# Performance work log

Measured on AMD Instinct MI355X. Metric: run time of the kernel, lower is better.

Reference implementation:

```python
import jax, jax.numpy as jnp
import numpy as np

N_NODES = 50000
N_EDGES = 600000
IN_C = 128
HID = 128
OUT_C = 32
N_GRAPHS = 64


def setup_inputs() -> dict:
    key = jax.random.key(0)
    ks = jax.random.split(key, 12)
    x = jax.random.normal(ks[0], (N_NODES, IN_C), dtype=jnp.float32)
    edge_index = jax.random.randint(ks[1], (2, N_EDGES), 0, N_NODES, dtype=jnp.int64)
    batch = jnp.sort(jax.random.randint(ks[2], (N_NODES,), 0, N_GRAPHS, dtype=jnp.int64))
    s1 = 1.0 / np.sqrt(IN_C)
    s2 = 1.0 / np.sqrt(HID)
    # SAGEConv: out = lin_l(mean_neighbors) + lin_r(x); lin_l has bias, lin_r has none
    W1l = jax.random.uniform(ks[3], (HID, IN_C), minval=-s1, maxval=s1, dtype=jnp.float32)
    b1 = jax.random.uniform(ks[4], (HID,), minval=-s1, maxval=s1, dtype=jnp.float32)
    W1r = jax.random.uniform(ks[5], (HID, IN_C), minval=-s1, maxval=s1, dtype=jnp.float32)
    W2l = jax.random.uniform(ks[6], (HID, HID), minval=-s2, maxval=s2, dtype=jnp.float32)
    b2 = jax.random.uniform(ks[7], (HID,), minval=-s2, maxval=s2, dtype=jnp.float32)
    W2r = jax.random.uniform(ks[8], (HID, HID), minval=-s2, maxval=s2, dtype=jnp.float32)
    Wlin = jax.random.uniform(ks[9], (OUT_C, HID), minval=-s2, maxval=s2, dtype=jnp.float32)
    blin = jax.random.uniform(ks[10], (OUT_C,), minval=-s2, maxval=s2, dtype=jnp.float32)
    return {"x": x, "edge_index": edge_index, "batch": batch,
            "W1l": W1l, "b1": b1, "W1r": W1r,
            "W2l": W2l, "b2": b2, "W2r": W2r,
            "Wlin": Wlin, "blin": blin}


def _sage_conv(x, src, dst, Wl, bl, Wr):
    # mean aggregation of source-node features onto destination nodes
    msg_sum = jax.ops.segment_sum(x[src], dst, num_segments=N_NODES)  # [N, d]
    deg = jax.ops.segment_sum(jnp.ones((src.shape[0],), x.dtype), dst, num_segments=N_NODES)
    mean = msg_sum / jnp.maximum(deg, 1.0)[:, None]
    return mean @ Wl.T + bl + x @ Wr.T


def reference(x, edge_index, batch, W1l, b1, W1r, W2l, b2, W2r, Wlin, blin):
    src, dst = edge_index[0], edge_index[1]
    h = jax.nn.relu(_sage_conv(x, src, dst, W1l, b1, W1r))
    h = jax.nn.relu(_sage_conv(h, src, dst, W2l, b2, W2r))
    # global mean pool over graph ids
    gsum = jax.ops.segment_sum(h, batch, num_segments=N_GRAPHS)        # [G, HID]
    cnt = jax.ops.segment_sum(jnp.ones((h.shape[0],), h.dtype), batch, num_segments=N_GRAPHS)
    pooled = gsum / jnp.maximum(cnt, 1.0)[:, None]
    return pooled @ Wlin.T + blin
```

## Files before the change

### kernel.cpp

```cpp
#include <hip/hip_runtime.h>
#include <hip/hip_fp16.h>

#define N_NODES 50000
#define N_EDGES 600000
#define N_GRAPHS 64
#define HID 128
#define OUT_C 32

#define N_SCAN_BLOCKS ((N_NODES + 255) / 256)
#define SCAN_FLAG 0x40000000

typedef __attribute__((ext_vector_type(8))) _Float16 half8;
typedef __attribute__((ext_vector_type(4))) float f32x4;

#define ZERO_INTS (2 * N_NODES + N_SCAN_BLOCKS)

__global__ __launch_bounds__(256) void prep_kernel(
    const float* __restrict__ x, const int* __restrict__ batch,
    const float* __restrict__ W1l, const float* __restrict__ W1r,
    const float* __restrict__ W2l, const float* __restrict__ W2r,
    __half* __restrict__ xh, __half* __restrict__ Wt1, __half* __restrict__ Wt2,
    int* __restrict__ zero_base, int* __restrict__ gstart) {
    const int b = blockIdx.x;
    const int t = threadIdx.x;
    const int gtid = b * 256 + t;
    const int gsz = gridDim.x * 256;
    for (int i = gtid; i < ZERO_INTS; i += gsz) zero_base[i] = 0;

    for (int i = gtid; i <= N_NODES; i += gsz) {
        if (i == 0) {
            int b1 = batch[0];
            for (int g = 0; g <= b1; ++g) gstart[g] = 0;
        } else if (i == N_NODES) {
            int b0 = batch[N_NODES - 1];
            for (int g = b0 + 1; g <= N_GRAPHS; ++g) gstart[g] = N_NODES;
        } else {
            int b0 = batch[i - 1], b1 = batch[i];
            for (int g = b0 + 1; g <= b1; ++g) gstart[g] = i;
        }
    }

    if (b < 16) {
        for (int i = gtid; i < 65536; i += 4096) {
            int which = i >> 15;
            int j = i & 32767;
            int n = j >> 8, k = j & 255;
            const float* Wl = which ? W2l : W1l;
            const float* Wr = which ? W2r : W1r;
            float a = (k < 128) ? Wl[n * 128 + k] : Wr[n * 128 + (k - 128)];
            (which ? Wt2 : Wt1)[j] = __float2half(a);
        }
    } else {
        int i = ((b - 16) * 256 + t) * 4;
        if (i < N_NODES * 128) {
            float4 v = *(const float4*)(x + i);
            __half2 a = __floats2half2_rn(v.x, v.y);
            __half2 c = __floats2half2_rn(v.z, v.w);
            uint2 st;
            st.x = *(const unsigned int*)&a;
            st.y = *(const unsigned int*)&c;
            *(uint2*)(xh + i) = st;
        }
    }
}

__global__ void deg_kernel(const int* __restrict__ dst, int* __restrict__ deg, int E) {
    int e = blockIdx.x * 256 + threadIdx.x;
    if (e < E) atomicAdd(&deg[dst[e]], 1);
}

__global__ __launch_bounds__(256) void scan_fused(
    const int* __restrict__ deg, int* __restrict__ bsum,
    int* __restrict__ rowptr, float* __restrict__ invdeg) {
    __shared__ int s[256];
    const int b = blockIdx.x;
    const int t = threadIdx.x;
    const int idx = b * 256 + t;
    const int v = (idx < N_NODES) ? deg[idx] : 0;
    s[t] = v;
    __syncthreads();
    for (int off = 1; off < 256; off <<= 1) {
        int u = (t >= off) ? s[t - off] : 0;
        __syncthreads();
        s[t] += u;
        __syncthreads();
    }
    const int incl = s[t];
    if (t == 255) atomicExch(&bsum[b], incl | SCAN_FLAG);

    int pv = 0;
    if (t < b) {
        int w;
        do { w = atomicAdd(&bsum[t], 0); } while (!(w & SCAN_FLAG));
        pv = w & ~SCAN_FLAG;
    }
    __syncthreads();
    s[t] = pv;
    __syncthreads();
    for (int off = 128; off > 0; off >>= 1) {
        if (t < off) s[t] += s[t + off];
        __syncthreads();
    }
    const int boffs = s[0];

    if (idx < N_NODES) {
        rowptr[idx] = boffs + incl - v;
        invdeg[idx] = 1.0f / fmaxf((float)v, 1.0f);
    }
    if (b == N_SCAN_BLOCKS - 1 && t == 255) rowptr[N_NODES] = boffs + incl;
}

__global__ void fill_kernel(const int* __restrict__ src, const int* __restrict__ dst,
                            const int* __restrict__ rowptr, int* __restrict__ cursor,
                            int* __restrict__ eidx, int E) {
    int e = blockIdx.x * 256 + threadIdx.x;
    if (e < E) {
        int d = dst[e];
        int pos = atomicAdd(&cursor[d], 1);
        eidx[rowptr[d] + pos] = src[e];
    }
}

#define AGG8(vv, aa, ab) { aa.x += (float)vv[0]; aa.y += (float)vv[1]; \
                           aa.z += (float)vv[2]; aa.w += (float)vv[3]; \
                           ab.x += (float)vv[4]; ab.y += (float)vv[5]; \
                           ab.z += (float)vv[6]; ab.w += (float)vv[7]; }

__global__ __launch_bounds__(256) void aggregate_f16(
    const __half* __restrict__ feat16, const int* __restrict__ rowptr,
    const int* __restrict__ eidx, const float* __restrict__ invdeg,
    __half* __restrict__ mean16) {
    const int wave = threadIdx.x >> 6;
    const int lane = threadIdx.x & 63;
    const int nh   = lane >> 4;
    const int sub  = lane & 15;
    const int node = blockIdx.x * 16 + wave * 4 + nh;
    const bool act = (node < N_NODES);
    int beg = 0, end = 0;
    if (act) { beg = rowptr[node]; end = rowptr[node + 1]; }
    const size_t coff = (size_t)sub * 8;

    float4 a0 = {0.f,0.f,0.f,0.f}, b0 = {0.f,0.f,0.f,0.f};
    float4 a1 = {0.f,0.f,0.f,0.f}, b1 = {0.f,0.f,0.f,0.f};
    float4 a2 = {0.f,0.f,0.f,0.f}, b2 = {0.f,0.f,0.f,0.f};
    float4 a3 = {0.f,0.f,0.f,0.f}, b3 = {0.f,0.f,0.f,0.f};
    int i = beg;
    for (; i + 8 <= end; i += 8) {
        int s0 = eidx[i+0], s1 = eidx[i+1], s2 = eidx[i+2], s3 = eidx[i+3];
        int s4 = eidx[i+4], s5 = eidx[i+5], s6 = eidx[i+6], s7 = eidx[i+7];
        half8 v0 = *(const half8*)(feat16 + (size_t)s0 * 128 + coff);
        half8 v1 = *(const half8*)(feat16 + (size_t)s1 * 128 + coff);
        half8 v2 = *(const half8*)(feat16 + (size_t)s2 * 128 + coff);
        half8 v3 = *(const half8*)(feat16 + (size_t)s3 * 128 + coff);
        half8 v4 = *(const half8*)(feat16 + (size_t)s4 * 128 + coff);
        half8 v5 = *(const half8*)(feat16 + (size_t)s5 * 128 + coff);
        half8 v6 = *(const half8*)(feat16 + (size_t)s6 * 128 + coff);
        half8 v7 = *(const half8*)(feat16 + (size_t)s7 * 128 + coff);
        AGG8(v0, a0, b0); AGG8(v1, a1, b1); AGG8(v2, a2, b2); AGG8(v3, a3, b3);
        AGG8(v4, a0, b0); AGG8(v5, a1, b1); AGG8(v6, a2, b2); AGG8(v7, a3, b3);
    }
    if (i + 4 <= end) {
        int s0 = eidx[i+0], s1 = eidx[i+1], s2 = eidx[i+2], s3 = eidx[i+3];
        half8 v0 = *(const half8*)(feat16 + (size_t)s0 * 128 + coff);
        half8 v1 = *(const half8*)(feat16 + (size_t)s1 * 128 + coff);
        half8 v2 = *(const half8*)(feat16 + (size_t)s2 * 128 + coff);
        half8 v3 = *(const half8*)(feat16 + (size_t)s3 * 128 + coff);
        AGG8(v0, a0, b0); AGG8(v1, a1, b1); AGG8(v2, a2, b2); AGG8(v3, a3, b3);
        i += 4;
    }
    if (i + 2 <= end) {
        int s0 = eidx[i+0], s1 = eidx[i+1];
        half8 v0 = *(const half8*)(feat16 + (size_t)s0 * 128 + coff);
        half8 v1 = *(const half8*)(feat16 + (size_t)s1 * 128 + coff);
        AGG8(v0, a0, b0); AGG8(v1, a1, b1);
        i += 2;
    }
    if (i < end) {
        int s0 = eidx[i];
        half8 v0 = *(const half8*)(feat16 + (size_t)s0 * 128 + coff);
        AGG8(v0, a0, b0);
    }

    if (act) {
        const float sc = invdeg[node];
        half8 r;
        r[0] = (_Float16)(((a0.x + a1.x) + (a2.x + a3.x)) * sc);
        r[1] = (_Float16)(((a0.y + a1.y) + (a2.y + a3.y)) * sc);
        r[2] = (_Float16)(((a0.z + a1.z) + (a2.z + a3.z)) * sc);
        r[3] = (_Float16)(((a0.w + a1.w) + (a2.w + a3.w)) * sc);
        r[4] = (_Float16)(((b0.x + b1.x) + (b2.x + b3.x)) * sc);
        r[5] = (_Float16)(((b0.y + b1.y) + (b2.y + b3.y)) * sc);
        r[6] = (_Float16)(((b0.z + b1.z) + (b2.z + b3.z)) * sc);
        r[7] = (_Float16)(((b0.w + b1.w) + (b2.w + b3.w)) * sc);
        *(half8*)(mean16 + (size_t)node * 128 + coff) = r;
    }
}

#define GBM 64
#define BPAD 8

__global__ __launch_bounds__(256) void sage_gemm_f16(
    const __half* __restrict__ mean16, const __half* __restrict__ feat16,
    const __half* __restrict__ Wt, const float* __restrict__ bias,
    __half* __restrict__ out16, int M) {
    __shared__ __align__(16) __half Bs[128][256 + BPAD];

    const int tid = threadIdx.x;
    const int wave = tid >> 6;
    const int lane = tid & 63;
    const int l15 = lane & 15;
    const int quad = lane >> 4;
    const int row0 = blockIdx.x * GBM;
    const int gi_a = min(row0 + wave * 16 + l15, M - 1);

    for (int id = tid; id < 128 * 32; id += 256) {
        int n = id >> 5;
        int kc = (id & 31) * 8;
        *(half8*)&Bs[n][kc] = *(const half8*)(Wt + (size_t)n * 256 + kc);
    }

    half8 af[8];
#pragma unroll
    for (int kb = 0; kb < 8; ++kb) {
        const int k0 = kb * 32;
        const __half* ap = (k0 < 128)
            ? (mean16 + (size_t)gi_a * 128 + k0 + quad * 8)
            : (feat16 + (size_t)gi_a * 128 + (k0 - 128) + quad * 8);
        af[kb] = *(const half8*)ap;
    }

    f32x4 acc[8];
#pragma unroll
    for (int t = 0; t < 8; ++t) acc[t] = (f32x4){0.f, 0.f, 0.f, 0.f};

    __syncthreads();

#pragma unroll
    for (int kb = 0; kb < 8; ++kb) {
#pragma unroll
        for (int t = 0; t < 8; ++t) {
            const half8 b = *(const half8*)&Bs[t * 16 + l15][kb * 32 + quad * 8];
            acc[t] = __builtin_amdgcn_mfma_f32_16x16x32_f16(af[kb], b, acc[t], 0, 0, 0);
        }
    }

#pragma unroll
    for (int r = 0; r < 4; ++r) {
        int gi = row0 + wave * 16 + quad * 4 + r;
        if (gi < M) {
#pragma unroll
            for (int t = 0; t < 8; ++t) {
                int col = t * 16 + l15;
                float v = fmaxf(acc[t][r] + bias[col], 0.f);
                out16[(size_t)gi * 128 + col] = __float2half(v);
            }
        }
    }
}

#define POOL_PARTS 4
__global__ __launch_bounds__(256) void pool_parts(
    const __half* __restrict__ h, const int* __restrict__ gstart,
    float* __restrict__ pooled_parts) {
    const int g = blockIdx.x >> 2;
    const int part = blockIdx.x & 3;
    const int start = gstart[g];
    const int end = gstart[g + 1];

    const int t = threadIdx.x;
    const int c4 = (t & 31) * 4;
    const int rg = t >> 5;
    float4 acc = {0.f, 0.f, 0.f, 0.f};
    for (int n = start + part * 8 + rg; n < end; n += 8 * POOL_PARTS) {
        const __half2* p = (const __half2*)(h + (size_t)n * 128 + c4);
        float2 f0 = __half22float2(p[0]);
        float2 f1 = __half22float2(p[1]);
        acc.x += f0.x; acc.y += f0.y; acc.z += f1.x; acc.w += f1.y;
    }
    __shared__ float sm[8][132];
    sm[rg][c4 + 0] = acc.x;
    sm[rg][c4 + 1] = acc.y;
    sm[rg][c4 + 2] = acc.z;
    sm[rg][c4 + 3] = acc.w;
    __syncthreads();
    if (t < 128) {
        float s = 0.f;
#pragma unroll
        for (int r = 0; r < 8; ++r) s += sm[r][t];
        pooled_parts[(size_t)blockIdx.x * 128 + t] = s;
    }
}

__global__ void final_kernel(const float* __restrict__ pooled_parts,
                             const int* __restrict__ gstart,
                             const float* __restrict__ Wlin, const float* __restrict__ blin,
                             float* __restrict__ out) {
    int g = blockIdx.x;
    int j = threadIdx.x;
    float inv = 1.0f / fmaxf((float)(gstart[g + 1] - gstart[g]), 1.0f);
    float sum = blin[j];
    const float* w = Wlin + j * 128;
    const float* p0 = pooled_parts + (size_t)(g * 4 + 0) * 128;
    const float* p1 = pooled_parts + (size_t)(g * 4 + 1) * 128;
    const float* p2 = pooled_parts + (size_t)(g * 4 + 2) * 128;
    const float* p3 = pooled_parts + (size_t)(g * 4 + 3) * 128;
    for (int c = 0; c < 128; ++c) {
        float p = (p0[c] + p1[c]) + (p2[c] + p3[c]);
        sum += p * inv * w[c];
    }
    out[g * 32 + j] = sum;
}

extern "C" void kernel_launch(void* const* d_in, const int* in_sizes, int n_in,
                              void* d_out, int out_size, void* d_ws, size_t ws_size,
                              hipStream_t stream) {
    const float* x    = (const float*)d_in[0];
    const int*   src  = (const int*)d_in[1];
    const int*   dst  = ((const int*)d_in[1]) + N_EDGES;
    const int*   batch= (const int*)d_in[2];
    const float* W1l  = (const float*)d_in[3];
    const float* b1   = (const float*)d_in[4];
    const float* W1r  = (const float*)d_in[5];
    const float* W2l  = (const float*)d_in[6];
    const float* b2   = (const float*)d_in[7];
    const float* W2r  = (const float*)d_in[8];
    const float* Wlin = (const float*)d_in[9];
    const float* blin = (const float*)d_in[10];
    float* out = (float*)d_out;

    __half* xh     = (__half*)d_ws;
    __half* mean16 = xh + 6400000;
    __half* h1_16  = mean16 + 6400000;
    __half* h2_16  = h1_16 + 6400000;
    __half* Wt1    = h2_16 + 6400000;
    __half* Wt2    = Wt1 + 32768;
    float* pooled_parts = (float*)(Wt2 + 32768);
    float* invdeg  = pooled_parts + 32768;
    int*   gstart  = (int*)(invdeg + N_NODES);
    int*   degi    = gstart + 65;
    int*   cursor  = degi + N_NODES;
    int*   bsum    = cursor + N_NODES;
    int*   rowptr  = bsum + N_SCAN_BLOCKS;
    int*   eidx    = rowptr + N_NODES + 1;

    prep_kernel<<<16 + (N_NODES * 128 / 4 + 255) / 256, 256, 0, stream>>>(
        x, batch, W1l, W1r, W2l, W2r, xh, Wt1, Wt2, degi, gstart);

    deg_kernel<<<(N_EDGES + 255) / 256, 256, 0, stream>>>(dst, degi, N_EDGES);
    scan_fused<<<N_SCAN_BLOCKS, 256, 0, stream>>>(degi, bsum, rowptr, invdeg);
    fill_kernel<<<(N_EDGES + 255) / 256, 256, 0, stream>>>(src, dst, rowptr, cursor, eidx, N_EDGES);

    const int gemm_grid = (N_NODES + GBM - 1) / GBM;
    const int agg_grid = (N_NODES + 15) / 16;

    aggregate_f16<<<agg_grid, 256, 0, stream>>>(xh, rowptr, eidx, invdeg, mean16);
    sage_gemm_f16<<<gemm_grid, 256, 0, stream>>>(mean16, xh, Wt1, b1, h1_16, N_NODES);

    aggregate_f16<<<agg_grid, 256, 0, stream>>>(h1_16, rowptr, eidx, invdeg, mean16);
    sage_gemm_f16<<<gemm_grid, 256, 0, stream>>>(mean16, h1_16, Wt2, b2, h2_16, N_NODES);

    pool_parts<<<N_GRAPHS * POOL_PARTS, 256, 0, stream>>>(h2_16, gstart, pooled_parts);
    final_kernel<<<N_GRAPHS, 32, 0, stream>>>(pooled_parts, gstart, Wlin, blin, out);
}
```

Before: 258.3 us.

## Fuse neighbor aggregation into SAGE GEMM via shared-memory A tile

Measured after the change: 311.1 us. 20.4% more time.

```diff
diff --git a/kernel.cpp b/kernel.cpp
--- a/kernel.cpp
+++ b/kernel.cpp
@@ -13,7 +13,7 @@
 typedef __attribute__((ext_vector_type(8))) _Float16 half8;
 typedef __attribute__((ext_vector_type(4))) float f32x4;
 
-#define ZERO_INTS (2 * N_NODES + N_SCAN_BLOCKS)
+#define ZERO_INTS (N_NODES + N_SCAN_BLOCKS)
 
 __global__ __launch_bounds__(256) void prep_kernel(
     const float* __restrict__ x, const int* __restrict__ batch,
@@ -71,7 +71,7 @@
 
 __global__ __launch_bounds__(256) void scan_fused(
     const int* __restrict__ deg, int* __restrict__ bsum,
-    int* __restrict__ rowptr, float* __restrict__ invdeg) {
+    int* __restrict__ rowptr, int* __restrict__ cursor, float* __restrict__ invdeg) {
     __shared__ int s[256];
     const int b = blockIdx.x;
     const int t = threadIdx.x;
@@ -104,85 +104,101 @@
     const int boffs = s[0];
 
     if (idx < N_NODES) {
-        rowptr[idx] = boffs + incl - v;
+        int rp = boffs + incl - v;
+        rowptr[idx] = rp;
+        cursor[idx] = rp;
         invdeg[idx] = 1.0f / fmaxf((float)v, 1.0f);
     }
     if (b == N_SCAN_BLOCKS - 1 && t == 255) rowptr[N_NODES] = boffs + incl;
 }
 
 __global__ void fill_kernel(const int* __restrict__ src, const int* __restrict__ dst,
-                            const int* __restrict__ rowptr, int* __restrict__ cursor,
-                            int* __restrict__ eidx, int E) {
+                            int* __restrict__ cursor, int* __restrict__ eidx, int E) {
     int e = blockIdx.x * 256 + threadIdx.x;
     if (e < E) {
-        int d = dst[e];
-        int pos = atomicAdd(&cursor[d], 1);
-        eidx[rowptr[d] + pos] = src[e];
-    }
-}
+        int pos = atomicAdd(&cursor[dst[e]], 1);
+        eidx[pos] = src[e];
+    }
+}
+
+#define GBM 64
+#define ALD 136
 
 #define AGG8(vv, aa, ab) { aa.x += (float)vv[0]; aa.y += (float)vv[1]; \
                            aa.z += (float)vv[2]; aa.w += (float)vv[3]; \
                            ab.x += (float)vv[4]; ab.y += (float)vv[5]; \
                            ab.z += (float)vv[6]; ab.w += (float)vv[7]; }
 
-__global__ __launch_bounds__(256) void aggregate_f16(
+__global__ __launch_bounds__(256) void sage_layer_f16(
     const __half* __restrict__ feat16, const int* __restrict__ rowptr,
     const int* __restrict__ eidx, const float* __restrict__ invdeg,
-    __half* __restrict__ mean16) {
-    const int wave = threadIdx.x >> 6;
-    const int lane = threadIdx.x & 63;
-    const int nh   = lane >> 4;
-    const int sub  = lane & 15;
-    const int node = blockIdx.x * 16 + wave * 4 + nh;
-    const bool act = (node < N_NODES);
-    int beg = 0, end = 0;
-    if (act) { beg = rowptr[node]; end = rowptr[node + 1]; }
-    const size_t coff = (size_t)sub * 8;
-
-    float4 a0 = {0.f,0.f,0.f,0.f}, b0 = {0.f,0.f,0.f,0.f};
-    float4 a1 = {0.f,0.f,0.f,0.f}, b1 = {0.f,0.f,0.f,0.f};
-    float4 a2 = {0.f,0.f,0.f,0.f}, b2 = {0.f,0.f,0.f,0.f};
-    float4 a3 = {0.f,0.f,0.f,0.f}, b3 = {0.f,0.f,0.f,0.f};
-    int i = beg;
-    for (; i + 8 <= end; i += 8) {
-        int s0 = eidx[i+0], s1 = eidx[i+1], s2 = eidx[i+2], s3 = eidx[i+3];
-        int s4 = eidx[i+4], s5 = eidx[i+5], s6 = eidx[i+6], s7 = eidx[i+7];
-        half8 v0 = *(const half8*)(feat16 + (size_t)s0 * 128 + coff);
-        half8 v1 = *(const half8*)(feat16 + (size_t)s1 * 128 + coff);
-        half8 v2 = *(const half8*)(feat16 + (size_t)s2 * 128 + coff);
-        half8 v3 = *(const half8*)(feat16 + (size_t)s3 * 128 + coff);
-        half8 v4 = *(const half8*)(feat16 + (size_t)s4 * 128 + coff);
-        half8 v5 = *(const half8*)(feat16 + (size_t)s5 * 128 + coff);
-        half8 v6 = *(const half8*)(feat16 + (size_t)s6 * 128 + coff);
-        half8 v7 = *(const half8*)(feat16 + (size_t)s7 * 128 + coff);
-        AGG8(v0, a0, b0); AGG8(v1, a1, b1); AGG8(v2, a2, b2); AGG8(v3, a3, b3);
-        AGG8(v4, a0, b0); AGG8(v5, a1, b1); AGG8(v6, a2, b2); AGG8(v7, a3, b3);
-    }
-    if (i + 4 <= end) {
-        int s0 = eidx[i+0], s1 = eidx[i+1], s2 = eidx[i+2], s3 = eidx[i+3];
-        half8 v0 = *(const half8*)(feat16 + (size_t)s0 * 128 + coff);
-        half8 v1 = *(const half8*)(feat16 + (size_t)s1 * 128 + coff);
-        half8 v2 = *(const half8*)(feat16 + (size_t)s2 * 128 + coff);
-        half8 v3 = *(const half8*)(feat16 + (size_t)s3 * 128 + coff);
-        AGG8(v0, a0, b0); AGG8(v1, a1, b1); AGG8(v2, a2, b2); AGG8(v3, a3, b3);
-        i += 4;
-    }
-    if (i + 2 <= end) {
-        int s0 = eidx[i+0], s1 = eidx[i+1];
-        half8 v0 = *(const half8*)(feat16 + (size_t)s0 * 128 + coff);
-        half8 v1 = *(const half8*)(feat16 + (size_t)s1 * 128 + coff);
-        AGG8(v0, a0, b0); AGG8(v1, a1, b1);
-        i += 2;
-    }
-    if (i < end) {
-        int s0 = eidx[i];
-        half8 v0 = *(const half8*)(feat16 + (size_t)s0 * 128 + coff);
-        AGG8(v0, a0, b0);
-    }
-
-    if (act) {
-        const float sc = invdeg[node];
+    const __half* __restrict__ Wt, const float* __restrict__ bias,
+    __half* __restrict__ out16, int M) {
+    __shared__ __align__(16) __half As[GBM][ALD];
+
+    const int tid = threadIdx.x;
+    const int wave = tid >> 6;
+    const int lane = tid & 63;
+    const int l15 = lane & 15;
+    const int quad = lane >> 4;
+    const int row0 = blockIdx.x * GBM;
+    const size_t coff = (size_t)l15 * 8;
+
+    const int gi_a = min(row0 + wave * 16 + l15, M - 1);
+    half8 af_hi[4];
+#pragma unroll
+    for (int kb = 0; kb < 4; ++kb)
+        af_hi[kb] = *(const half8*)(feat16 + (size_t)gi_a * 128 + kb * 32 + quad * 8);
+
+    for (int p = 0; p < 4; ++p) {
+        const int lrow = wave * 16 + p * 4 + quad;
+        const int node = row0 + lrow;
+        const bool act = (node < M);
+        int beg = 0, end = 0;
+        if (act) { beg = rowptr[node]; end = rowptr[node + 1]; }
+
+        float4 a0 = {0.f,0.f,0.f,0.f}, b0 = {0.f,0.f,0.f,0.f};
+        float4 a1 = {0.f,0.f,0.f,0.f}, b1 = {0.f,0.f,0.f,0.f};
+        float4 a2 = {0.f,0.f,0.f,0.f}, b2 = {0.f,0.f,0.f,0.f};
+        float4 a3 = {0.f,0.f,0.f,0.f}, b3 = {0.f,0.f,0.f,0.f};
+        int i = beg;
+        for (; i + 8 <= end; i += 8) {
+            int s0 = eidx[i+0], s1 = eidx[i+1], s2 = eidx[i+2], s3 = eidx[i+3];
+            int s4 = eidx[i+4], s5 = eidx[i+5], s6 = eidx[i+6], s7 = eidx[i+7];
+            half8 v0 = *(const half8*)(feat16 + (size_t)s0 * 128 + coff);
+            half8 v1 = *(const half8*)(feat16 + (size_t)s1 * 128 + coff);
+            half8 v2 = *(const half8*)(feat16 + (size_t)s2 * 128 + coff);
+            half8 v3 = *(const half8*)(feat16 + (size_t)s3 * 128 + coff);
+            half8 v4 = *(const half8*)(feat16 + (size_t)s4 * 128 + coff);
+            half8 v5 = *(const half8*)(feat16 + (size_t)s5 * 128 + coff);
+            half8 v6 = *(const half8*)(feat16 + (size_t)s6 * 128 + coff);
+            half8 v7 = *(const half8*)(feat16 + (size_t)s7 * 128 + coff);
+            AGG8(v0, a0, b0); AGG8(v1, a1, b1); AGG8(v2, a2, b2); AGG8(v3, a3, b3);
+            AGG8(v4, a0, b0); AGG8(v5, a1, b1); AGG8(v6, a2, b2); AGG8(v7, a3, b3);
+        }
+        if (i + 4 <= end) {
+            int s0 = eidx[i+0], s1 = eidx[i+1], s2 = eidx[i+2], s3 = eidx[i+3];
+            half8 v0 = *(const half8*)(feat16 + (size_t)s0 * 128 + coff);
+            half8 v1 = *(const half8*)(feat16 + (size_t)s1 * 128 + coff);
+            half8 v2 = *(const half8*)(feat16 + (size_t)s2 * 128 + coff);
+            half8 v3 = *(const half8*)(feat16 + (size_t)s3 * 128 + coff);
+            AGG8(v0, a0, b0); AGG8(v1, a1, b1); AGG8(v2, a2, b2); AGG8(v3, a3, b3);
+            i += 4;
+        }
+        if (i + 2 <= end) {
+            int s0 = eidx[i+0], s1 = eidx[i+1];
+            half8 v0 = *(const half8*)(feat16 + (size_t)s0 * 128 + coff);
+            half8 v1 = *(const half8*)(feat16 + (size_t)s1 * 128 + coff);
+            AGG8(v0, a0, b0); AGG8(v1, a1, b1);
+            i += 2;
+        }
+        if (i < end) {
+            int s0 = eidx[i];
+            half8 v0 = *(const half8*)(feat16 + (size_t)s0 * 128 + coff);
+            AGG8(v0, a0, b0);
+        }
+
+        const float sc = act ? invdeg[node] : 0.0f;
         half8 r;
         r[0] = (_Float16)(((a0.x + a1.x) + (a2.x + a3.x)) * sc);
         r[1] = (_Float16)(((a0.y + a1.y) + (a2.y + a3.y)) * sc);
@@ -192,55 +208,23 @@
         r[5] = (_Float16)(((b0.y + b1.y) + (b2.y + b3.y)) * sc);
         r[6] = (_Float16)(((b0.z + b1.z) + (b2.z + b3.z)) * sc);
         r[7] = (_Float16)(((b0.w + b1.w) + (b2.w + b3.w)) * sc);
-        *(half8*)(mean16 + (size_t)node * 128 + coff) = r;
-    }
-}
-
-#define GBM 64
-#define BPAD 8
-
-__global__ __launch_bounds__(256) void sage_gemm_f16(
-    const __half* __restrict__ mean16, const __half* __restrict__ feat16,
-    const __half* __restrict__ Wt, const float* __restrict__ bias,
-    __half* __restrict__ out16, int M) {
-    __shared__ __align__(16) __half Bs[128][256 + BPAD];
-
-    const int tid = threadIdx.x;
-    const int wave = tid >> 6;
-    const int lane = tid & 63;
-    const int l15 = lane & 15;
-    const int quad = lane >> 4;
-    const int row0 = blockIdx.x * GBM;
-    const int gi_a = min(row0 + wave * 16 + l15, M - 1);
-
-    for (int id = tid; id < 128 * 32; id += 256) {
-        int n = id >> 5;
-        int kc = (id & 31) * 8;
-        *(half8*)&Bs[n][kc] = *(const half8*)(Wt + (size_t)n * 256 + kc);
-    }
-
-    half8 af[8];
+        *(half8*)&As[lrow][l15 * 8] = r;
+    }
+
+    __syncthreads();
+
+    f32x4 acc[8];
+#pragma unroll
+    for (int t = 0; t < 8; ++t) acc[t] = (f32x4){0.f, 0.f, 0.f, 0.f};
+
 #pragma unroll
     for (int kb = 0; kb < 8; ++kb) {
-        const int k0 = kb * 32;
-        const __half* ap = (k0 < 128)
-            ? (mean16 + (size_t)gi_a * 128 + k0 + quad * 8)
-            : (feat16 + (size_t)gi_a * 128 + (k0 - 128) + quad * 8);
-        af[kb] = *(const half8*)ap;
-    }
-
-    f32x4 acc[8];
-#pragma unroll
-    for (int t = 0; t < 8; ++t) acc[t] = (f32x4){0.f, 0.f, 0.f, 0.f};
-
-    __syncthreads();
-
-#pragma unroll
-    for (int kb = 0; kb < 8; ++kb) {
+        const half8 a = (kb < 4) ? *(const half8*)&As[wave * 16 + l15][kb * 32 + quad * 8]
+                                 : af_hi[kb - 4];
 #pragma unroll
         for (int t = 0; t < 8; ++t) {
-            const half8 b = *(const half8*)&Bs[t * 16 + l15][kb * 32 + quad * 8];
-            acc[t] = __builtin_amdgcn_mfma_f32_16x16x32_f16(af[kb], b, acc[t], 0, 0, 0);
+            const half8 b = *(const half8*)(Wt + (size_t)(t * 16 + l15) * 256 + kb * 32 + quad * 8);
+            acc[t] = __builtin_amdgcn_mfma_f32_16x16x32_f16(a, b, acc[t], 0, 0, 0);
         }
     }
 
@@ -329,8 +313,7 @@
     float* out = (float*)d_out;
 
     __half* xh     = (__half*)d_ws;
-    __half* mean16 = xh + 6400000;
-    __half* h1_16  = mean16 + 6400000;
+    __half* h1_16  = xh + 6400000;
     __half* h2_16  = h1_16 + 6400000;
     __half* Wt1    = h2_16 + 6400000;
     __half* Wt2    = Wt1 + 32768;
@@ -338,26 +321,22 @@
     float* invdeg  = pooled_parts + 32768;
     int*   gstart  = (int*)(invdeg + N_NODES);
     int*   degi    = gstart + 65;
-    int*   cursor  = degi + N_NODES;
-    int*   bsum    = cursor + N_NODES;
-    int*   rowptr  = bsum + N_SCAN_BLOCKS;
+    int*   bsum    = degi + N_NODES;
+    int*   cursor  = bsum + N_SCAN_BLOCKS;
+    int*   rowptr  = cursor + N_NODES;
     int*   eidx    = rowptr + N_NODES + 1;
 
     prep_kernel<<<16 + (N_NODES * 128 / 4 + 255) / 256, 256, 0, stream>>>(
         x, batch, W1l, W1r, W2l, W2r, xh, Wt1, Wt2, degi, gstart);
 
     deg_kernel<<<(N_EDGES + 255) / 256, 256, 0, stream>>>(dst, degi, N_EDGES);
-    scan_fused<<<N_SCAN_BLOCKS, 256, 0, stream>>>(degi, bsum, rowptr, invdeg);
-    fill_kernel<<<(N_EDGES + 255) / 256, 256, 0, stream>>>(src, dst, rowptr, cursor, eidx, N_EDGES);
-
-    const int gemm_grid = (N_NODES + GBM - 1) / GBM;
-    const int agg_grid = (N_NODES + 15) / 16;
-
-    aggregate_f16<<<agg_grid, 256, 0, stream>>>(xh, rowptr, eidx, invdeg, mean16);
-    sage_gemm_f16<<<gemm_grid, 256, 0, stream>>>(mean16, xh, Wt1, b1, h1_16, N_NODES);
-
-    aggregate_f16<<<agg_grid, 256, 0, stream>>>(h1_16, rowptr, eidx, invdeg, mean16);
-    sage_gemm_f16<<<gemm_grid, 256, 0, stream>>>(mean16, h1_16, Wt2, b2, h2_16, N_NODES);
+    scan_fused<<<N_SCAN_BLOCKS, 256, 0, stream>>>(degi, bsum, rowptr, cursor, invdeg);
+    fill_kernel<<<(N_EDGES + 255) / 256, 256, 0, stream>>>(src, dst, cursor, eidx, N_EDGES);
+
+    const int layer_grid = (N_NODES + GBM - 1) / GBM;
+
+    sage_layer_f16<<<layer_grid, 256, 0, stream>>>(xh, rowptr, eidx, invdeg, Wt1, b1, h1_16, N_NODES);
+    sage_layer_f16<<<layer_grid, 256, 0, stream>>>(h1_16, rowptr, eidx, invdeg, Wt2, b2, h2_16, N_NODES);
 
     pool_parts<<<N_GRAPHS * POOL_PARTS, 256, 0, stream>>>(h2_16, gstart, pooled_parts);
     final_kernel<<<N_GRAPHS, 32, 0, stream>>>(pooled_parts, gstart, Wlin, blin, out);
```

## Fuse global mean pooling into second SAGE GEMM epilogue and simplify CSR fill

Applied to the files above, without the earlier changes.

Measured after the change: 322.0 us. 1.25x slower.

```diff
diff --git a/kernel.cpp b/kernel.cpp
--- a/kernel.cpp
+++ b/kernel.cpp
@@ -13,7 +13,7 @@
 typedef __attribute__((ext_vector_type(8))) _Float16 half8;
 typedef __attribute__((ext_vector_type(4))) float f32x4;
 
-#define ZERO_INTS (2 * N_NODES + N_SCAN_BLOCKS)
+#define ZERO_INTS (N_GRAPHS * 128 + N_NODES + N_SCAN_BLOCKS)
 
 __global__ __launch_bounds__(256) void prep_kernel(
     const float* __restrict__ x, const int* __restrict__ batch,
@@ -71,7 +71,7 @@
 
 __global__ __launch_bounds__(256) void scan_fused(
     const int* __restrict__ deg, int* __restrict__ bsum,
-    int* __restrict__ rowptr, float* __restrict__ invdeg) {
+    int* __restrict__ rowptr, int* __restrict__ cursor, float* __restrict__ invdeg) {
     __shared__ int s[256];
     const int b = blockIdx.x;
     const int t = threadIdx.x;
@@ -104,20 +104,20 @@
     const int boffs = s[0];
 
     if (idx < N_NODES) {
-        rowptr[idx] = boffs + incl - v;
+        int rp = boffs + incl - v;
+        rowptr[idx] = rp;
+        cursor[idx] = rp;
         invdeg[idx] = 1.0f / fmaxf((float)v, 1.0f);
     }
     if (b == N_SCAN_BLOCKS - 1 && t == 255) rowptr[N_NODES] = boffs + incl;
 }
 
 __global__ void fill_kernel(const int* __restrict__ src, const int* __restrict__ dst,
-                            const int* __restrict__ rowptr, int* __restrict__ cursor,
-                            int* __restrict__ eidx, int E) {
+                            int* __restrict__ cursor, int* __restrict__ eidx, int E) {
     int e = blockIdx.x * 256 + threadIdx.x;
     if (e < E) {
-        int d = dst[e];
-        int pos = atomicAdd(&cursor[d], 1);
-        eidx[rowptr[d] + pos] = src[e];
+        int pos = atomicAdd(&cursor[dst[e]], 1);
+        eidx[pos] = src[e];
     }
 }
 
@@ -197,13 +197,13 @@
 }
 
 #define GBM 64
-#define BPAD 8
 
 __global__ __launch_bounds__(256) void sage_gemm_f16(
     const __half* __restrict__ mean16, const __half* __restrict__ feat16,
     const __half* __restrict__ Wt, const float* __restrict__ bias,
-    __half* __restrict__ out16, int M) {
-    __shared__ __align__(16) __half Bs[128][256 + BPAD];
+    const int* __restrict__ batch, __half* __restrict__ out16,
+    float* __restrict__ pooled, int M) {
+    __shared__ float pool_lds[8][128];
 
     const int tid = threadIdx.x;
     const int wave = tid >> 6;
@@ -213,10 +213,8 @@
     const int row0 = blockIdx.x * GBM;
     const int gi_a = min(row0 + wave * 16 + l15, M - 1);
 
-    for (int id = tid; id < 128 * 32; id += 256) {
-        int n = id >> 5;
-        int kc = (id & 31) * 8;
-        *(half8*)&Bs[n][kc] = *(const half8*)(Wt + (size_t)n * 256 + kc);
+    if (pooled) {
+        for (int i = tid; i < 8 * 128; i += 256) pool_lds[i >> 7][i & 127] = 0.f;
     }
 
     half8 af[8];
@@ -233,65 +231,56 @@
 #pragma unroll
     for (int t = 0; t < 8; ++t) acc[t] = (f32x4){0.f, 0.f, 0.f, 0.f};
 
-    __syncthreads();
+    if (pooled) __syncthreads();
 
 #pragma unroll
     for (int kb = 0; kb < 8; ++kb) {
 #pragma unroll
         for (int t = 0; t < 8; ++t) {
-            const half8 b = *(const half8*)&Bs[t * 16 + l15][kb * 32 + quad * 8];
+            const half8 b = *(const half8*)(Wt + (size_t)(t * 16 + l15) * 256 + kb * 32 + quad * 8);
             acc[t] = __builtin_amdgcn_mfma_f32_16x16x32_f16(af[kb], b, acc[t], 0, 0, 0);
         }
     }
 
-#pragma unroll
-    for (int r = 0; r < 4; ++r) {
-        int gi = row0 + wave * 16 + quad * 4 + r;
-        if (gi < M) {
-#pragma unroll
-            for (int t = 0; t < 8; ++t) {
-                int col = t * 16 + l15;
-                float v = fmaxf(acc[t][r] + bias[col], 0.f);
-                out16[(size_t)gi * 128 + col] = __float2half(v);
+    if (pooled) {
+        const int gmin = batch[row0];
+#pragma unroll
+        for (int r = 0; r < 4; ++r) {
+            int gi = row0 + wave * 16 + quad * 4 + r;
+            if (gi < M) {
+                int gl = batch[gi] - gmin;
+#pragma unroll
+                for (int t = 0; t < 8; ++t) {
+                    int col = t * 16 + l15;
+                    float v = fmaxf(acc[t][r] + bias[col], 0.f);
+                    if (gl < 8) atomicAdd(&pool_lds[gl][col], v);
+                    else        atomicAdd(&pooled[(gmin + gl) * 128 + col], v);
+                }
             }
         }
-    }
-}
-
-#define POOL_PARTS 4
-__global__ __launch_bounds__(256) void pool_parts(
-    const __half* __restrict__ h, const int* __restrict__ gstart,
-    float* __restrict__ pooled_parts) {
-    const int g = blockIdx.x >> 2;
-    const int part = blockIdx.x & 3;
-    const int start = gstart[g];
-    const int end = gstart[g + 1];
-
-    const int t = threadIdx.x;
-    const int c4 = (t & 31) * 4;
-    const int rg = t >> 5;
-    float4 acc = {0.f, 0.f, 0.f, 0.f};
-    for (int n = start + part * 8 + rg; n < end; n += 8 * POOL_PARTS) {
-        const __half2* p = (const __half2*)(h + (size_t)n * 128 + c4);
-        float2 f0 = __half22float2(p[0]);
-        float2 f1 = __half22float2(p[1]);
-        acc.x += f0.x; acc.y += f0.y; acc.z += f1.x; acc.w += f1.y;
-    }
-    __shared__ float sm[8][132];
-    sm[rg][c4 + 0] = acc.x;
-    sm[rg][c4 + 1] = acc.y;
-    sm[rg][c4 + 2] = acc.z;
-    sm[rg][c4 + 3] = acc.w;
-    __syncthreads();
-    if (t < 128) {
-        float s = 0.f;
-#pragma unroll
-        for (int r = 0; r < 8; ++r) s += sm[r][t];
-        pooled_parts[(size_t)blockIdx.x * 128 + t] = s;
-    }
-}
-
-__global__ void final_kernel(const float* __restrict__ pooled_parts,
+        __syncthreads();
+        for (int i = tid; i < 8 * 128; i += 256) {
+            int gl = i >> 7, c = i & 127;
+            float v = pool_lds[gl][c];
+            if (v != 0.f) atomicAdd(&pooled[(gmin + gl) * 128 + c], v);
+        }
+    } else {
+#pragma unroll
+        for (int r = 0; r < 4; ++r) {
+            int gi = row0 + wave * 16 + quad * 4 + r;
+            if (gi < M) {
+#pragma unroll
+                for (int t = 0; t < 8; ++t) {
+                    int col = t * 16 + l15;
+                    float v = fmaxf(acc[t][r] + bias[col], 0.f);
+                    out16[(size_t)gi * 128 + col] = __float2half(v);
+                }
+            }
+        }
+    }
+}
+
+__global__ void final_kernel(const float* __restrict__ pooled,
                              const int* __restrict__ gstart,
                              const float* __restrict__ Wlin, const float* __restrict__ blin,
                              float* __restrict__ out) {
@@ -300,14 +289,8 @@
     float inv = 1.0f / fmaxf((float)(gstart[g + 1] - gstart[g]), 1.0f);
     float sum = blin[j];
     const float* w = Wlin + j * 128;
-    const float* p0 = pooled_parts + (size_t)(g * 4 + 0) * 128;
-    const float* p1 = pooled_parts + (size_t)(g * 4 + 1) * 128;
-    const float* p2 = pooled_parts + (size_t)(g * 4 + 2) * 128;
-    const float* p3 = pooled_parts + (size_t)(g * 4 + 3) * 128;
-    for (int c = 0; c < 128; ++c) {
-        float p = (p0[c] + p1[c]) + (p2[c] + p3[c]);
-        sum += p * inv * w[c];
-    }
+    const float* p = pooled + (size_t)g * 128;
+    for (int c = 0; c < 128; ++c) sum += p[c] * inv * w[c];
     out[g * 32 + j] = sum;
 }
 
@@ -331,34 +314,34 @@
     __half* xh     = (__half*)d_ws;
     __half* mean16 = xh + 6400000;
     __half* h1_16  = mean16 + 6400000;
-    __half* h2_16  = h1_16 + 6400000;
-    __half* Wt1    = h2_16 + 6400000;
+    __half* Wt1    = h1_16 + 6400000;
     __half* Wt2    = Wt1 + 32768;
-    float* pooled_parts = (float*)(Wt2 + 32768);
-    float* invdeg  = pooled_parts + 32768;
+    float* invdeg  = (float*)(Wt2 + 32768);
     int*   gstart  = (int*)(invdeg + N_NODES);
-    int*   degi    = gstart + 65;
-    int*   cursor  = degi + N_NODES;
-    int*   bsum    = cursor + N_NODES;
-    int*   rowptr  = bsum + N_SCAN_BLOCKS;
+    float* pooled  = (float*)(gstart + 65);
+    int*   degi    = (int*)(pooled + N_GRAPHS * 128);
+    int*   bsum    = degi + N_NODES;
+    int*   cursor  = bsum + N_SCAN_BLOCKS;
+    int*   rowptr  = cursor + N_NODES;
     int*   eidx    = rowptr + N_NODES + 1;
 
     prep_kernel<<<16 + (N_NODES * 128 / 4 + 255) / 256, 256, 0, stream>>>(
-        x, batch, W1l, W1r, W2l, W2r, xh, Wt1, Wt2, degi, gstart);
+        x, batch, W1l, W1r, W2l, W2r, xh, Wt1, Wt2, (int*)pooled, gstart);
 
     deg_kernel<<<(N_EDGES + 255) / 256, 256, 0, stream>>>(dst, degi, N_EDGES);
-    scan_fused<<<N_SCAN_BLOCKS, 256, 0, stream>>>(degi, bsum, rowptr, invdeg);
-    fill_kernel<<<(N_EDGES + 255) / 256, 256, 0, stream>>>(src, dst, rowptr, cursor, eidx, N_EDGES);
+    scan_fused<<<N_SCAN_BLOCKS, 256, 0, stream>>>(degi, bsum, rowptr, cursor, invdeg);
+    fill_kernel<<<(N_EDGES + 255) / 256, 256, 0, stream>>>(src, dst, cursor, eidx, N_EDGES);
 
     const int gemm_grid = (N_NODES + GBM - 1) / GBM;
     const int agg_grid = (N_NODES + 15) / 16;
 
     aggregate_f16<<<agg_grid, 256, 0, stream>>>(xh, rowptr, eidx, invdeg, mean16);
-    sage_gemm_f16<<<gemm_grid, 256, 0, stream>>>(mean16, xh, Wt1, b1, h1_16, N_NODES);
+    sage_gemm_f16<<<gemm_grid, 256, 0, stream>>>(mean16, xh, Wt1, b1, batch,
+                                                 h1_16, (float*)nullptr, N_NODES);
 
     aggregate_f16<<<agg_grid, 256, 0, stream>>>(h1_16, rowptr, eidx, invdeg, mean16);
-    sage_gemm_f16<<<gemm_grid, 256, 0, stream>>>(mean16, h1_16, Wt2, b2, h2_16, N_NODES);
-
-    pool_parts<<<N_GRAPHS * POOL_PARTS, 256, 0, stream>>>(h2_16, gstart, pooled_parts);
-    final_kernel<<<N_GRAPHS, 32, 0, stream>>>(pooled_parts, gstart, Wlin, blin, out);
-}
+    sage_gemm_f16<<<gemm_grid, 256, 0, stream>>>(mean16, h1_16, Wt2, b2, batch,
+                                                 (__half*)nullptr, pooled, N_NODES);
+
+    final_kernel<<<N_GRAPHS, 32, 0, stream>>>(pooled, gstart, Wlin, blin, out);
+}
```
